# Kernel optimization log

Measured on AMD Instinct MI355X. Metric: run time of the kernel, lower is better.

The kernel has to match this reference:

```python
import jax, jax.numpy as jnp
import numpy as np
from jax import lax

LN_EPS = 1e-5

def _conv1d(h, w, b):
    # h: [N, L, Cin], w: [Cout, Cin, K] (torch Conv1d layout), padding=1
    out = lax.conv_general_dilated(h, w, window_strides=(1,), padding=[(1, 1)],
                                   dimension_numbers=("NWC", "OIW", "NWC"))
    return out + b

def _layer_norm(h, g, b):
    m = jnp.mean(h, axis=-1, keepdims=True)
    v = jnp.mean((h - m) ** 2, axis=-1, keepdims=True)
    return (h - m) * lax.rsqrt(v + LN_EPS) * g + b

def setup_inputs() -> dict:
    key = jax.random.key(0)
    ks = jax.random.split(key, 8)
    N, L, D, F = 32, 512, 384, 256
    return {
        "x": jax.random.normal(ks[0], (N, L, D), jnp.float32),
        "conv1_w": jax.random.normal(ks[1], (F, D, 3), jnp.float32) * 0.05,
        "conv1_b": jnp.zeros((F,), jnp.float32),
        "ln1_g": jnp.ones((F,), jnp.float32),
        "ln1_b": jnp.zeros((F,), jnp.float32),
        "conv2_w": jax.random.normal(ks[2], (F, F, 3), jnp.float32) * 0.05,
        "conv2_b": jnp.zeros((F,), jnp.float32),
        "ln2_g": jnp.ones((F,), jnp.float32),
        "ln2_b": jnp.zeros((F,), jnp.float32),
        "lin_w": jax.random.normal(ks[3], (F,), jnp.float32) * 0.05,
        "lin_b": jnp.zeros((), jnp.float32),
        "target": jax.random.randint(ks[4], (N, L), 0, 8, dtype=jnp.int32),
        "mel_max_length": 2048,
    }

def reference(x, conv1_w, conv1_b, ln1_g, ln1_b, conv2_w, conv2_b, ln2_g, ln2_b,
              lin_w, lin_b, target, mel_max_length):
    # Duration predictor (dropout is identity at inference)
    h = jax.nn.relu(_layer_norm(_conv1d(x, conv1_w, conv1_b), ln1_g, ln1_b))
    h = jax.nn.relu(_layer_norm(_conv1d(h, conv2_w, conv2_b), ln2_g, ln2_b))
    duration_predictor_output = jnp.einsum("nlf,f->nl", h, lin_w) + lin_b  # [N, L]

    # LR: frame t copies phoneme j iff cumsum(dur)[:j] <= t < cumsum(dur)[:j+1]
    # (equivalent to the one-hot alignment matmul, padded to mel_max_length)
    N, L, D = x.shape
    T = mel_max_length
    cums = jnp.cumsum(target, axis=-1)                      # [N, L]
    frames = jnp.arange(T, dtype=cums.dtype)                # [T]
    idx = jax.vmap(lambda c: jnp.searchsorted(c, frames, side="right"))(cums)  # [N, T]
    valid = frames[None, :] < cums[:, -1:]                  # frames beyond total are zero
    gathered = jnp.take_along_axis(x, jnp.clip(idx, 0, L - 1)[:, :, None], axis=1)
    output = gathered * valid[:, :, None].astype(x.dtype)   # [N, T, D]
    return output, duration_predictor_output
```

## Files before the change

### kernel.cpp

```cpp
#include <hip/hip_runtime.h>
#include <hip/hip_bf16.h>

typedef unsigned short u16;
typedef short s8v __attribute__((ext_vector_type(8)));
typedef float f4v __attribute__((ext_vector_type(4)));
typedef u16 u16x8 __attribute__((ext_vector_type(8)));

static __device__ __forceinline__ u16 f2bf(float v) {
    __hip_bfloat16 h = __float2bfloat16(v);
    return *(u16*)&h;
}

__global__ __launch_bounds__(256) void gather_prep_kernel(
    const float* __restrict__ x,
    const int*   __restrict__ target,
    const float* __restrict__ w1,
    const float* __restrict__ w2,
    u16* __restrict__ Wt1,
    u16* __restrict__ Wt2,
    float* __restrict__ out0)
{
    __shared__ int c[512];
    __shared__ int ridx[64];
    const int b = blockIdx.x, tid = threadIdx.x;

    if (b >= 1024) {
        if (b < 2176) {
            const int K = 1152, DIN = 384;
            int e = (b - 1024) * 256 + tid;
            int f = e / K;
            int rem = e - f * K;
            int kc = rem / DIN;
            int d = rem - kc * DIN;
            Wt1[e] = f2bf(w1[f * K + d * 3 + kc]);
        } else {
            const int K = 768, DIN = 256;
            int e = (b - 2176) * 256 + tid;
            int f = e / K;
            int rem = e - f * K;
            int kc = rem / DIN;
            int d = rem - kc * DIN;
            Wt2[e] = f2bf(w2[f * K + d * 3 + kc]);
        }
        return;
    }

    const int n = b >> 5, sub = b & 31;
    c[tid]       = target[n * 512 + tid];
    c[tid + 256] = target[n * 512 + 256 + tid];
    __syncthreads();
    for (int off = 1; off < 512; off <<= 1) {
        int v0 = (tid       >= off) ? c[tid       - off] : 0;
        int v1 = (tid + 256 >= off) ? c[tid + 256 - off] : 0;
        __syncthreads();
        c[tid]       += v0;
        c[tid + 256] += v1;
        __syncthreads();
    }
    const int total = c[511];
    if (tid < 64) {
        int t = sub * 64 + tid;
        int lo = 0, hi = 512;
        while (lo < hi) {
            int mid = (lo + hi) >> 1;
            if (c[mid] <= t) lo = mid + 1; else hi = mid;
        }
        ridx[tid] = (t < total) ? min(lo, 511) : -1;
    }
    __syncthreads();

    const size_t xbase = (size_t)(n << 9) * 384;
    const size_t obase = ((size_t)(n << 11) + sub * 64) * 384;
    #pragma unroll 4
    for (int it = 0; it < 12; ++it) {
        int u  = tid + it * 256;
        int j  = u % 48;
        int rl = u / 48;
        int ie = ridx[rl];
        f4v v0 = {0.f, 0.f, 0.f, 0.f}, v1 = v0;
        if (ie >= 0) {
            const float* src = &x[xbase + (size_t)ie * 384];
            v0 = *(const f4v*)&src[j * 4];
            v1 = *(const f4v*)&src[(j + 48) * 4];
        }
        float* dst = &out0[obase + (size_t)rl * 384];
        __builtin_nontemporal_store(v0, (f4v*)&dst[j * 4]);
        __builtin_nontemporal_store(v1, (f4v*)&dst[(j + 48) * 4]);
    }
}

__global__ __launch_bounds__(256, 2) void fused_conv_kernel(
    const float* __restrict__ x,
    const u16* __restrict__ Wt1,
    const u16* __restrict__ Wt2,
    const float* __restrict__ cb1, const float* __restrict__ g1,
    const float* __restrict__ bb1,
    const float* __restrict__ cb2, const float* __restrict__ g2,
    const float* __restrict__ bb2,
    const float* __restrict__ lw, const float* __restrict__ lbp,
    float* __restrict__ dpo)
{
    __shared__ __align__(128) char LDS[73216];
    char* Bs    = LDS + 38400;
    float* redS = (float*)(LDS + 71168);
    float* redQ = (float*)(LDS + 71936);
    float* redP = (float*)(LDS + 72704);

    const int tid  = threadIdx.x;
    const int lane = tid & 63, wc = tid >> 6;
    const int lr = lane & 15, q4 = lane >> 4;
    const int sb = (blockIdx.x & 7) * 64 + (blockIdx.x >> 3);
    const int m0 = sb * 32;
    const int n  = m0 >> 9, l0 = m0 & 511;

    const int b_r    = tid >> 3;
    const int b_slot = (tid & 7) ^ (b_r & 7);
    int boff[4];
    #pragma unroll
    for (int ni = 0; ni < 4; ni++) boff[ni] = (64 * wc + 16 * ni + lr) * 128;
    const int slot0 = ((q4)     ^ (lr & 7)) << 4;
    const int slot1 = ((q4 | 4) ^ (lr & 7)) << 4;

    for (int u = tid; u < 2400; u += 256) {
        int j = u / 48, s = u - j * 48;
        int lp = l0 - 9 + j;
        f4v v0 = {0.f, 0.f, 0.f, 0.f}, v1 = v0;
        if (lp >= 0 && lp < 512) {
            const float* src = x + ((size_t)((n << 9) + lp)) * 384 + s * 8;
            v0 = *(const f4v*)src;
            v1 = *(const f4v*)(src + 4);
        }
        u16x8 r;
        #pragma unroll
        for (int jj = 0; jj < 4; jj++) { r[jj] = f2bf(v0[jj]); r[4 + jj] = f2bf(v1[jj]); }
        int ss = (s & ~7) | ((s & 7) ^ (j & 7));
        *(u16x8*)(LDS + j * 768 + ss * 16) = r;
    }

    auto xwread = [&](int j, int s) -> s8v {
        int ss = (s & ~7) | ((s & 7) ^ (j & 7));
        return *(const s8v*)(LDS + j * 768 + (ss << 4));
    };

    f4v acc[3][4];
    #pragma unroll
    for (int mi = 0; mi < 3; mi++)
        #pragma unroll
        for (int ni = 0; ni < 4; ni++) acc[mi][ni] = {0.f, 0.f, 0.f, 0.f};

    for (int t = 0; t < 18; ++t) {
        __syncthreads();
        const int k0 = t * 64;
        const u16* bsrc = Wt1 + (size_t)b_r * 1152 + k0 + b_slot * 8;
        #pragma unroll
        for (int q = 0; q < 8; q++) {
            __builtin_amdgcn_global_load_lds(
                (const __attribute__((address_space(1))) void*)(bsrc + (size_t)q * 32 * 1152),
                (__attribute__((address_space(3))) void*)(Bs + q * 4096 + tid * 16),
                16, 0, 0);
        }
        __syncthreads();

        const int kc = k0 / 384;
        const int s0 = (k0 - kc * 384) >> 3;
        #pragma unroll
        for (int kk = 0; kk < 2; kk++) {
            const int sl = kk ? slot1 : slot0;
            const int s  = s0 + 4 * kk + q4;
            s8v a0 = xwread(lr + kc,      s);
            s8v a1 = xwread(16 + lr + kc, s);
            s8v a2 = xwread(32 + lr + kc, s);
            s8v b0 = *(const s8v*)(Bs + boff[0] + sl);
            s8v b1 = *(const s8v*)(Bs + boff[1] + sl);
            s8v b2 = *(const s8v*)(Bs + boff[2] + sl);
            s8v b3 = *(const s8v*)(Bs + boff[3] + sl);
            acc[0][0] = __builtin_amdgcn_mfma_f32_16x16x32_bf16(a0, b0, acc[0][0], 0, 0, 0);
            acc[0][1] = __builtin_amdgcn_mfma_f32_16x16x32_bf16(a0, b1, acc[0][1], 0, 0, 0);
            acc[0][2] = __builtin_amdgcn_mfma_f32_16x16x32_bf16(a0, b2, acc[0][2], 0, 0, 0);
            acc[0][3] = __builtin_amdgcn_mfma_f32_16x16x32_bf16(a0, b3, acc[0][3], 0, 0, 0);
            acc[1][0] = __builtin_amdgcn_mfma_f32_16x16x32_bf16(a1, b0, acc[1][0], 0, 0, 0);
            acc[1][1] = __builtin_amdgcn_mfma_f32_16x16x32_bf16(a1, b1, acc[1][1], 0, 0, 0);
            acc[1][2] = __builtin_amdgcn_mfma_f32_16x16x32_bf16(a1, b2, acc[1][2], 0, 0, 0);
            acc[1][3] = __builtin_amdgcn_mfma_f32_16x16x32_bf16(a1, b3, acc[1][3], 0, 0, 0);
            acc[2][0] = __builtin_amdgcn_mfma_f32_16x16x32_bf16(a2, b0, acc[2][0], 0, 0, 0);
            acc[2][1] = __builtin_amdgcn_mfma_f32_16x16x32_bf16(a2, b1, acc[2][1], 0, 0, 0);
            acc[2][2] = __builtin_amdgcn_mfma_f32_16x16x32_bf16(a2, b2, acc[2][2], 0, 0, 0);
            acc[2][3] = __builtin_amdgcn_mfma_f32_16x16x32_bf16(a2, b3, acc[2][3], 0, 0, 0);
        }
    }

    int col[4];
    float cbv[4], gv[4], bbv[4];
    #pragma unroll
    for (int ni = 0; ni < 4; ni++) {
        col[ni] = 64 * wc + 16 * ni + lr;
        cbv[ni] = cb1[col[ni]]; gv[ni] = g1[col[ni]]; bbv[ni] = bb1[col[ni]];
    }

    #pragma unroll
    for (int mi = 0; mi < 3; mi++)
        #pragma unroll
        for (int reg = 0; reg < 4; reg++) {
            float s = 0.f, q = 0.f;
            #pragma unroll
            for (int ni = 0; ni < 4; ni++) {
                float v = acc[mi][ni][reg] + cbv[ni];
                s += v; q += v * v;
            }
            #pragma unroll
            for (int msk = 1; msk < 16; msk <<= 1) {
                s += __shfl_xor(s, msk);
                q += __shfl_xor(q, msk);
            }
            if (lr == 0) {
                int rl = 16 * mi + 4 * q4 + reg;
                redS[rl * 4 + wc] = s;
                redQ[rl * 4 + wc] = q;
            }
        }
    __syncthreads();

    #pragma unroll
    for (int mi = 0; mi < 3; mi++)
        #pragma unroll
        for (int reg = 0; reg < 4; reg++) {
            int rl = 16 * mi + 4 * q4 + reg;
            int h  = rl - 7;
            if (h >= 0 && h < 34) {
                float4 ps = *(float4*)&redS[rl * 4];
                float4 pq = *(float4*)&redQ[rl * 4];
                float mean = (ps.x + ps.y + ps.z + ps.w) * (1.f / 256.f);
                float var  = (pq.x + pq.y + pq.z + pq.w) * (1.f / 256.f) - mean * mean;
                float rs   = rsqrtf(var + 1e-5f);
                int l = l0 - 8 + rl;
                bool lv = (l >= 0 && l < 512);
                #pragma unroll
                for (int ni = 0; ni < 4; ni++) {
                    float v = acc[mi][ni][reg] + cbv[ni];
                    float o = lv ? fmaxf(0.f, (v - mean) * rs * gv[ni] + bbv[ni]) : 0.f;
                    int slot = (col[ni] >> 3) ^ (h & 7);
                    *(u16*)(LDS + h * 512 + slot * 16 + (col[ni] & 7) * 2) = f2bf(o);
                }
            }
        }

    f4v acc2[2][4];
    #pragma unroll
    for (int mi = 0; mi < 2; mi++)
        #pragma unroll
        for (int ni = 0; ni < 4; ni++) acc2[mi][ni] = {0.f, 0.f, 0.f, 0.f};

    for (int t2 = 0; t2 < 12; ++t2) {
        __syncthreads();
        const int k0 = t2 * 64;
        const u16* bsrc = Wt2 + (size_t)b_r * 768 + k0 + b_slot * 8;
        #pragma unroll
        for (int q = 0; q < 8; q++) {
            __builtin_amdgcn_global_load_lds(
                (const __attribute__((address_space(1))) void*)(bsrc + (size_t)q * 32 * 768),
                (__attribute__((address_space(3))) void*)(Bs + q * 4096 + tid * 16),
                16, 0, 0);
        }
        __syncthreads();

        const int kc2   = t2 >> 2;
        const int sbase = 8 * (t2 & 3);
        #pragma unroll
        for (int kk = 0; kk < 2; kk++) {
            const int sl = kk ? slot1 : slot0;
            s8v b0 = *(const s8v*)(Bs + boff[0] + sl);
            s8v b1 = *(const s8v*)(Bs + boff[1] + sl);
            s8v b2 = *(const s8v*)(Bs + boff[2] + sl);
            s8v b3 = *(const s8v*)(Bs + boff[3] + sl);
            s8v a0, a1;
            {
                int h = lr + kc2;
                int s = sbase + 4 * kk + q4;
                a0 = *(const s8v*)(LDS + h * 512 + ((s ^ (h & 7)) << 4));
                h = 16 + lr + kc2;
                a1 = *(const s8v*)(LDS + h * 512 + ((s ^ (h & 7)) << 4));
            }
            acc2[0][0] = __builtin_amdgcn_mfma_f32_16x16x32_bf16(a0, b0, acc2[0][0], 0, 0, 0);
            acc2[0][1] = __builtin_amdgcn_mfma_f32_16x16x32_bf16(a0, b1, acc2[0][1], 0, 0, 0);
            acc2[0][2] = __builtin_amdgcn_mfma_f32_16x16x32_bf16(a0, b2, acc2[0][2], 0, 0, 0);
            acc2[0][3] = __builtin_amdgcn_mfma_f32_16x16x32_bf16(a0, b3, acc2[0][3], 0, 0, 0);
            acc2[1][0] = __builtin_amdgcn_mfma_f32_16x16x32_bf16(a1, b0, acc2[1][0], 0, 0, 0);
            acc2[1][1] = __builtin_amdgcn_mfma_f32_16x16x32_bf16(a1, b1, acc2[1][1], 0, 0, 0);
            acc2[1][2] = __builtin_amdgcn_mfma_f32_16x16x32_bf16(a1, b2, acc2[1][2], 0, 0, 0);
            acc2[1][3] = __builtin_amdgcn_mfma_f32_16x16x32_bf16(a1, b3, acc2[1][3], 0, 0, 0);
        }
    }

    float cbv2[4], gv2[4], bbv2[4], lwv[4];
    #pragma unroll
    for (int ni = 0; ni < 4; ni++) {
        cbv2[ni] = cb2[col[ni]]; gv2[ni] = g2[col[ni]]; bbv2[ni] = bb2[col[ni]];
        lwv[ni]  = lw[col[ni]];
    }

    float sv[2][4], sq[2][4];
    #pragma unroll
    for (int mi = 0; mi < 2; mi++)
        #pragma unroll
        for (int reg = 0; reg < 4; reg++) {
            float s = 0.f, q = 0.f;
            #pragma unroll
            for (int ni = 0; ni < 4; ni++) {
                float v = acc2[mi][ni][reg] + cbv2[ni];
                s += v; q += v * v;
            }
            #pragma unroll
            for (int msk = 1; msk < 16; msk <<= 1) {
                s += __shfl_xor(s, msk);
                q += __shfl_xor(q, msk);
            }
            sv[mi][reg] = s; sq[mi][reg] = q;
        }
    __syncthreads();
    if (lr == 0) {
        #pragma unroll
        for (int mi = 0; mi < 2; mi++)
            #pragma unroll
            for (int reg = 0; reg < 4; reg++) {
                int rl = 16 * mi + 4 * q4 + reg;
                redS[rl * 4 + wc] = sv[mi][reg];
                redQ[rl * 4 + wc] = sq[mi][reg];
            }
    }
    __syncthreads();

    float pp[2][4];
    #pragma unroll
    for (int mi = 0; mi < 2; mi++)
        #pragma unroll
        for (int reg = 0; reg < 4; reg++) {
            int rl = 16 * mi + 4 * q4 + reg;
            float4 ps = *(float4*)&redS[rl * 4];
            float4 pq = *(float4*)&redQ[rl * 4];
            float mean = (ps.x + ps.y + ps.z + ps.w) * (1.f / 256.f);
            float var  = (pq.x + pq.y + pq.z + pq.w) * (1.f / 256.f) - mean * mean;
            float rs   = rsqrtf(var + 1e-5f);
            float p = 0.f;
            #pragma unroll
            for (int ni = 0; ni < 4; ni++) {
                float v = acc2[mi][ni][reg] + cbv2[ni];
                float o = fmaxf(0.f, (v - mean) * rs * gv2[ni] + bbv2[ni]);
                p += o * lwv[ni];
            }
            #pragma unroll
            for (int msk = 1; msk < 16; msk <<= 1) p += __shfl_xor(p, msk);
            pp[mi][reg] = p;
        }
    if (lr == 0) {
        #pragma unroll
        for (int mi = 0; mi < 2; mi++)
            #pragma unroll
            for (int reg = 0; reg < 4; reg++) {
                int rl = 16 * mi + 4 * q4 + reg;
                redP[rl * 4 + wc] = pp[mi][reg];
            }
    }
    __syncthreads();
    if (tid < 32) {
        float4 p4 = *(float4*)&redP[tid * 4];
        dpo[m0 + tid] = p4.x + p4.y + p4.z + p4.w + lbp[0];
    }
}

extern "C" void kernel_launch(void* const* d_in, const int* in_sizes, int n_in,
                              void* d_out, int out_size, void* d_ws, size_t ws_size,
                              hipStream_t stream) {
    const float* x   = (const float*)d_in[0];
    const float* w1  = (const float*)d_in[1];
    const float* b1  = (const float*)d_in[2];
    const float* g1  = (const float*)d_in[3];
    const float* bb1 = (const float*)d_in[4];
    const float* w2  = (const float*)d_in[5];
    const float* b2  = (const float*)d_in[6];
    const float* g2  = (const float*)d_in[7];
    const float* bb2 = (const float*)d_in[8];
    const float* lw  = (const float*)d_in[9];
    const float* lb  = (const float*)d_in[10];
    const int* target = (const int*)d_in[11];

    char* wsb = (char*)d_ws;
    u16*  Wt1 = (u16*)wsb;
    u16*  Wt2 = (u16*)(wsb + 589824);

    float* out0 = (float*)d_out;
    float* dpo  = out0 + (size_t)32 * 2048 * 384;

    gather_prep_kernel<<<2944, 256, 0, stream>>>(
        x, target, w1, w2, Wt1, Wt2, out0);

    fused_conv_kernel<<<512, 256, 0, stream>>>(
        x, Wt1, Wt2, b1, g1, bb1, b2, g2, bb2, lw, lb, dpo);
}
```

Measured before the change: 67.65 us.

## Read conv weights directly from global memory and shrink the shared x halo tile

Drops the per-K-step staging of weight tiles into LDS through global_load_lds, along with the two barriers per iteration around it. Each wave now loads its weight fragments straight from global memory, relying on L2 to serve the reuse. The x tile is cut to only the 36 rows that actually hold data, and out-of-range rows are clamped in the reader. This lowers LDS use from about 72KB to 29KB, which could raise occupancy, but global-load latency now sits directly in front of the MFMA chain with no prefetch to hide it.

```diff
diff --git a/kernel.cpp b/kernel.cpp
--- a/kernel.cpp
+++ b/kernel.cpp
@@ -100,11 +100,10 @@
     const float* __restrict__ lw, const float* __restrict__ lbp,
     float* __restrict__ dpo)
 {
-    __shared__ __align__(128) char LDS[73216];
-    char* Bs    = LDS + 38400;
-    float* redS = (float*)(LDS + 71168);
-    float* redQ = (float*)(LDS + 71936);
-    float* redP = (float*)(LDS + 72704);
+    __shared__ __align__(128) char LDS[29696];
+    float* redS = (float*)(LDS + 27648);
+    float* redQ = (float*)(LDS + 28416);
+    float* redP = (float*)(LDS + 29184);
 
     const int tid  = threadIdx.x;
     const int lane = tid & 63, wc = tid >> 6;
@@ -113,17 +112,9 @@
     const int m0 = sb * 32;
     const int n  = m0 >> 9, l0 = m0 & 511;
 
-    const int b_r    = tid >> 3;
-    const int b_slot = (tid & 7) ^ (b_r & 7);
-    int boff[4];
-    #pragma unroll
-    for (int ni = 0; ni < 4; ni++) boff[ni] = (64 * wc + 16 * ni + lr) * 128;
-    const int slot0 = ((q4)     ^ (lr & 7)) << 4;
-    const int slot1 = ((q4 | 4) ^ (lr & 7)) << 4;
-
-    for (int u = tid; u < 2400; u += 256) {
-        int j = u / 48, s = u - j * 48;
-        int lp = l0 - 9 + j;
+    for (int u = tid; u < 1728; u += 256) {
+        int j7 = u / 48, s = u - j7 * 48;
+        int lp = l0 - 2 + j7;
         f4v v0 = {0.f, 0.f, 0.f, 0.f}, v1 = v0;
         if (lp >= 0 && lp < 512) {
             const float* src = x + ((size_t)((n << 9) + lp)) * 384 + s * 8;
@@ -133,15 +124,26 @@
         u16x8 r;
         #pragma unroll
         for (int jj = 0; jj < 4; jj++) { r[jj] = f2bf(v0[jj]); r[4 + jj] = f2bf(v1[jj]); }
-        int ss = (s & ~7) | ((s & 7) ^ (j & 7));
-        *(u16x8*)(LDS + j * 768 + ss * 16) = r;
-    }
+        int ss = (s & ~7) | ((s & 7) ^ (j7 & 7));
+        *(u16x8*)(LDS + j7 * 768 + ss * 16) = r;
+    }
+    __syncthreads();
 
     auto xwread = [&](int j, int s) -> s8v {
-        int ss = (s & ~7) | ((s & 7) ^ (j & 7));
-        return *(const s8v*)(LDS + j * 768 + (ss << 4));
+        int j7 = min(max(j, 7), 42) - 7;
+        int ss = (s & ~7) | ((s & 7) ^ (j7 & 7));
+        return *(const s8v*)(LDS + j7 * 768 + (ss << 4));
     };
 
+    const u16* b1row[4];
+    const u16* b2row[4];
+    #pragma unroll
+    for (int ni = 0; ni < 4; ni++) {
+        int row = 64 * wc + 16 * ni + lr;
+        b1row[ni] = Wt1 + (size_t)row * 1152;
+        b2row[ni] = Wt2 + (size_t)row * 768;
+    }
+
     f4v acc[3][4];
     #pragma unroll
     for (int mi = 0; mi < 3; mi++)
@@ -149,31 +151,20 @@
         for (int ni = 0; ni < 4; ni++) acc[mi][ni] = {0.f, 0.f, 0.f, 0.f};
 
     for (int t = 0; t < 18; ++t) {
-        __syncthreads();
         const int k0 = t * 64;
-        const u16* bsrc = Wt1 + (size_t)b_r * 1152 + k0 + b_slot * 8;
-        #pragma unroll
-        for (int q = 0; q < 8; q++) {
-            __builtin_amdgcn_global_load_lds(
-                (const __attribute__((address_space(1))) void*)(bsrc + (size_t)q * 32 * 1152),
-                (__attribute__((address_space(3))) void*)(Bs + q * 4096 + tid * 16),
-                16, 0, 0);
-        }
-        __syncthreads();
-
         const int kc = k0 / 384;
         const int s0 = (k0 - kc * 384) >> 3;
         #pragma unroll
         for (int kk = 0; kk < 2; kk++) {
-            const int sl = kk ? slot1 : slot0;
-            const int s  = s0 + 4 * kk + q4;
+            const int s    = s0 + 4 * kk + q4;
+            const int koff = k0 + (4 * kk + q4) * 8;
+            s8v b0 = *(const s8v*)(b1row[0] + koff);
+            s8v b1 = *(const s8v*)(b1row[1] + koff);
+            s8v b2 = *(const s8v*)(b1row[2] + koff);
+            s8v b3 = *(const s8v*)(b1row[3] + koff);
             s8v a0 = xwread(lr + kc,      s);
             s8v a1 = xwread(16 + lr + kc, s);
             s8v a2 = xwread(32 + lr + kc, s);
-            s8v b0 = *(const s8v*)(Bs + boff[0] + sl);
-            s8v b1 = *(const s8v*)(Bs + boff[1] + sl);
-            s8v b2 = *(const s8v*)(Bs + boff[2] + sl);
-            s8v b3 = *(const s8v*)(Bs + boff[3] + sl);
             acc[0][0] = __builtin_amdgcn_mfma_f32_16x16x32_bf16(a0, b0, acc[0][0], 0, 0, 0);
             acc[0][1] = __builtin_amdgcn_mfma_f32_16x16x32_bf16(a0, b1, acc[0][1], 0, 0, 0);
             acc[0][2] = __builtin_amdgcn_mfma_f32_16x16x32_bf16(a0, b2, acc[0][2], 0, 0, 0);
@@ -243,6 +234,7 @@
                 }
             }
         }
+    __syncthreads();
 
     f4v acc2[2][4];
     #pragma unroll
@@ -251,27 +243,15 @@
         for (int ni = 0; ni < 4; ni++) acc2[mi][ni] = {0.f, 0.f, 0.f, 0.f};
 
     for (int t2 = 0; t2 < 12; ++t2) {
-        __syncthreads();
-        const int k0 = t2 * 64;
-        const u16* bsrc = Wt2 + (size_t)b_r * 768 + k0 + b_slot * 8;
-        #pragma unroll
-        for (int q = 0; q < 8; q++) {
-            __builtin_amdgcn_global_load_lds(
-                (const __attribute__((address_space(1))) void*)(bsrc + (size_t)q * 32 * 768),
-                (__attribute__((address_space(3))) void*)(Bs + q * 4096 + tid * 16),
-                16, 0, 0);
-        }
-        __syncthreads();
-
         const int kc2   = t2 >> 2;
         const int sbase = 8 * (t2 & 3);
         #pragma unroll
         for (int kk = 0; kk < 2; kk++) {
-            const int sl = kk ? slot1 : slot0;
-            s8v b0 = *(const s8v*)(Bs + boff[0] + sl);
-            s8v b1 = *(const s8v*)(Bs + boff[1] + sl);
-            s8v b2 = *(const s8v*)(Bs + boff[2] + sl);
-            s8v b3 = *(const s8v*)(Bs + boff[3] + sl);
+            const int koff = t2 * 64 + (4 * kk + q4) * 8;
+            s8v b0 = *(const s8v*)(b2row[0] + koff);
+            s8v b1 = *(const s8v*)(b2row[1] + koff);
+            s8v b2 = *(const s8v*)(b2row[2] + koff);
+            s8v b3 = *(const s8v*)(b2row[3] + koff);
             s8v a0, a1;
             {
                 int h = lr + kc2;
```

Result: slower. 88.81 us (+31.3%).
